# Optimization experiments

Measured on AMD Instinct MI355X. Metric: run time of the kernel, lower is better.

## Reference

```python
import jax, jax.numpy as jnp
import numpy as np

B, S, D, H, FF = 2, 2048, 1024, 16, 4096
DK = D // H
EPS = 1e-6  # LayerNormalization eps


def setup_inputs() -> dict:
    key = jax.random.key(0)
    ks = jax.random.split(key, 12)
    n = lambda k, shp, s=0.02: (jax.random.normal(k, shp, jnp.float32) * s)
    z = lambda shp: jnp.zeros(shp, jnp.float32)
    return {
        "x": jax.random.normal(ks[0], (B, S, D), jnp.float32),
        # attention projections (torch Linear: weight [out, in], bias [out])
        "wq": n(ks[1], (D, D)), "bq": z((D,)),
        "wk": n(ks[2], (D, D)), "bk": z((D,)),
        "wv": n(ks[3], (D, D)), "bv": z((D,)),
        "wo": n(ks[4], (D, D)), "bo": z((D,)),
        # feed-forward
        "w1": n(ks[5], (FF, D)), "b1": z((FF,)),
        "w2": n(ks[6], (D, FF)), "b2": z((D,)),
        # custom LayerNormalization: scalar alpha (ones(1)) and bias (zeros(1))
        "ln1_a": jnp.ones((1,), jnp.float32), "ln1_b": z((1,)),
        "ln2_a": jnp.ones((1,), jnp.float32), "ln2_b": z((1,)),
        # original code path uses `if mask:` -> falsy None; represented as 0
        "src_mask": 0,
    }


def _layernorm(x, alpha, bias):
    # Faithful to source: alpha * (x - mean) / sqrt(std + eps) + bias,
    # with std the UNBIASED std (torch default) and sqrt applied to std itself.
    mean = jnp.mean(x, axis=-1, keepdims=True)
    std = jnp.std(x, axis=-1, keepdims=True, ddof=1)
    return alpha * (x - mean) / jnp.sqrt(std + EPS) + bias


def _mha(x, wq, bq, wk, bk, wv, bv, wo, bo):
    # x: (B, S, D)
    q = (jnp.einsum("bsd,ed->bse", x, wq) + bq).reshape(B, S, H, DK).transpose(0, 2, 1, 3)
    k = (jnp.einsum("bsd,ed->bse", x, wk) + bk).reshape(B, S, H, DK).transpose(0, 2, 1, 3)
    v = (jnp.einsum("bsd,ed->bse", x, wv) + bv).reshape(B, S, H, DK).transpose(0, 2, 1, 3)
    scores = jnp.einsum("bhqd,bhkd->bhqk", q, k) / jnp.sqrt(jnp.float32(DK))
    attn = jax.nn.softmax(scores, axis=-1)  # mask is None, dropout eval -> identity
    out = jnp.einsum("bhqk,bhkd->bhqd", attn, v)
    out = out.transpose(0, 2, 1, 3).reshape(B, S, D)
    return jnp.einsum("bsd,ed->bse", out, wo) + bo


def reference(x, wq, bq, wk, bk, wv, bv, wo, bo, w1, b1, w2, b2,
              ln1_a, ln1_b, ln2_a, ln2_b, src_mask):
    # residual 1: pre-norm self-attention
    h = x + _mha(_layernorm(x, ln1_a, ln1_b), wq, bq, wk, bk, wv, bv, wo, bo)
    # residual 2: pre-norm FFN (linear -> relu -> linear)
    hn = _layernorm(h, ln2_a, ln2_b)
    ffn = jnp.einsum("bsf,df->bsd", jax.nn.relu(jnp.einsum("bsd,fd->bsf", hn, w1) + b1), w2) + b2
    return h + ffn
```

## Files before the change

kernel.cpp:

```cpp
#include <hip/hip_runtime.h>
#include <stdint.h>

#define Bb 2
#define Ss 2048
#define Dd 1024
#define Hh 16
#define DKk 64
#define FFf 4096
#define Mm 4096
#define LN_EPS 1e-6f
#define QB 32
#define KVB 64

typedef __attribute__((ext_vector_type(8))) short bf16x8;
typedef __attribute__((ext_vector_type(4))) float f32x4;

__device__ __forceinline__ unsigned short f32_to_bf16(float f) {
  union { float f; uint32_t u; } v; v.f = f;
  uint32_t u = v.u;
  u += 0x7FFFu + ((u >> 16) & 1u);
  return (unsigned short)(u >> 16);
}

struct CastArgs {
  const float4* src[6];
  ushort4* dst[6];
  int cum[7];
};
__global__ __launch_bounds__(256) void cast_all(CastArgs a, int total4) {
  int stride = gridDim.x * blockDim.x;
  for (int i = blockIdx.x * blockDim.x + threadIdx.x; i < total4; i += stride) {
    int s = 0;
    #pragma unroll
    for (int k = 1; k < 6; ++k) s += (i >= a.cum[k]);
    float4 v = a.src[s][i - a.cum[s]];
    ushort4 o;
    o.x = f32_to_bf16(v.x); o.y = f32_to_bf16(v.y);
    o.z = f32_to_bf16(v.z); o.w = f32_to_bf16(v.w);
    a.dst[s][i - a.cum[s]] = o;
  }
}

__global__ __launch_bounds__(256) void layernorm_kernel(
    const float* __restrict__ x, const float* __restrict__ alpha_p,
    const float* __restrict__ bias_p, unsigned short* __restrict__ out)
{
  __shared__ float redS[4], redQ[4];
  int row = blockIdx.x, tid = threadIdx.x;
  const float4 v = ((const float4*)(x + (size_t)row * Dd))[tid];
  float s  = v.x + v.y + v.z + v.w;
  float sq = v.x*v.x + v.y*v.y + v.z*v.z + v.w*v.w;
  #pragma unroll
  for (int off = 32; off; off >>= 1) { s += __shfl_down(s, off); sq += __shfl_down(sq, off); }
  if ((tid & 63) == 0) { redS[tid >> 6] = s; redQ[tid >> 6] = sq; }
  __syncthreads();
  float S  = redS[0] + redS[1] + redS[2] + redS[3];
  float Qq = redQ[0] + redQ[1] + redQ[2] + redQ[3];
  float mean = S * (1.f / Dd);
  float var  = fmaxf((Qq - mean * S) * (1.f / (Dd - 1)), 0.f);
  float k    = alpha_p[0] / sqrtf(sqrtf(var) + LN_EPS);
  float bias = bias_p[0];
  ushort4 ov;
  ov.x = f32_to_bf16((v.x - mean) * k + bias);
  ov.y = f32_to_bf16((v.y - mean) * k + bias);
  ov.z = f32_to_bf16((v.z - mean) * k + bias);
  ov.w = f32_to_bf16((v.w - mean) * k + bias);
  ((ushort4*)(out + (size_t)row * Dd))[tid] = ov;
}

template<int FLAGS>
__global__ __launch_bounds__(256) void gemm_bt(
    const unsigned short* __restrict__ A,
    const unsigned short* __restrict__ W,
    const float* __restrict__ bias,
    const float* __restrict__ resid,
    void* __restrict__ Cout,
    int M, int N, int K)
{
  __shared__ unsigned short As[128 * 32];
  __shared__ unsigned short Bs[128 * 32];
  const int tid  = threadIdx.x;
  const int lane = tid & 63;
  const int wid  = tid >> 6;
  const int wr   = wid >> 1, wc = wid & 1;
  const int brow = blockIdx.y * 128;
  const int bcol = blockIdx.x * 128;
  const int lane15 = lane & 15;
  const int laneK8 = (lane >> 4) * 8;

  f32x4 acc[4][4] = {};

  for (int kk = 0; kk < K; kk += 32) {
    #pragma unroll
    for (int rnd = 0; rnd < 2; ++rnd) {
      int f   = rnd * 4096 + tid * 16;
      int row = f >> 6;
      int ce  = (f & 63) >> 1;
      const unsigned short* ga = A + (size_t)(brow + row) * K + kk + ce;
      const unsigned short* gw = W + (size_t)(bcol + row) * K + kk + ce;
      __builtin_amdgcn_global_load_lds((const __attribute__((address_space(1))) void*)ga,
          (__attribute__((address_space(3))) void*)&As[rnd * 2048 + wid * 512], 16, 0, 0);
      __builtin_amdgcn_global_load_lds((const __attribute__((address_space(1))) void*)gw,
          (__attribute__((address_space(3))) void*)&Bs[rnd * 2048 + wid * 512], 16, 0, 0);
    }
    __syncthreads();

    bf16x8 af[4], bfr[4];
    #pragma unroll
    for (int i = 0; i < 4; ++i) {
      af[i]  = *(const bf16x8*)&As[(wr * 64 + i * 16 + lane15) * 32 + laneK8];
      bfr[i] = *(const bf16x8*)&Bs[(wc * 64 + i * 16 + lane15) * 32 + laneK8];
    }
    #pragma unroll
    for (int i = 0; i < 4; ++i)
      #pragma unroll
      for (int j = 0; j < 4; ++j)
        acc[i][j] = __builtin_amdgcn_mfma_f32_16x16x32_bf16(af[i], bfr[j], acc[i][j], 0, 0, 0);
    __syncthreads();
  }

  #pragma unroll
  for (int i = 0; i < 4; ++i) {
    int row0 = brow + wr * 64 + i * 16 + (lane >> 4) * 4;
    #pragma unroll
    for (int j = 0; j < 4; ++j) {
      int col = bcol + wc * 64 + j * 16 + lane15;
      float bv = bias[col];
      #pragma unroll
      for (int r = 0; r < 4; ++r) {
        float v = acc[i][j][r] + bv;
        if (FLAGS & 1) v = fmaxf(v, 0.f);
        size_t idx = (size_t)(row0 + r) * N + col;
        if (FLAGS & 2) ((float*)Cout)[idx] = resid[idx] + v;
        else           ((unsigned short*)Cout)[idx] = f32_to_bf16(v);
      }
    }
  }
}

template<int FLAGS>
__global__ __launch_bounds__(256) void gemm_bt64(
    const unsigned short* __restrict__ A,
    const unsigned short* __restrict__ W,
    const float* __restrict__ bias,
    const float* __restrict__ resid,
    void* __restrict__ Cout,
    int M, int N, int K)
{
  __shared__ unsigned short As[64 * 64];
  __shared__ unsigned short Bs[128 * 64];
  const int tid  = threadIdx.x;
  const int lane = tid & 63;
  const int wid  = tid >> 6;
  const int wr   = wid >> 1, wc = wid & 1;
  const int brow = blockIdx.y * 64;
  const int bcol = blockIdx.x * 128;
  const int lane15 = lane & 15;
  const int lgb16  = (lane >> 4) * 16;

  f32x4 acc[2][4] = {};

  for (int kk = 0; kk < K; kk += 64) {
    #pragma unroll
    for (int rnd = 0; rnd < 2; ++rnd) {
      int p    = rnd * 4096 + tid * 16;
      int row  = p >> 7;
      int colu = ((p & 127) ^ ((row & 7) << 4)) >> 1;
      const unsigned short* ga = A + (size_t)(brow + row) * K + kk + colu;
      __builtin_amdgcn_global_load_lds((const __attribute__((address_space(1))) void*)ga,
          (__attribute__((address_space(3))) void*)&As[rnd * 2048 + wid * 512], 16, 0, 0);
    }
    #pragma unroll
    for (int rnd = 0; rnd < 4; ++rnd) {
      int p    = rnd * 4096 + tid * 16;
      int row  = p >> 7;
      int colu = ((p & 127) ^ ((row & 7) << 4)) >> 1;
      const unsigned short* gw = W + (size_t)(bcol + row) * K + kk + colu;
      __builtin_amdgcn_global_load_lds((const __attribute__((address_space(1))) void*)gw,
          (__attribute__((address_space(3))) void*)&Bs[rnd * 2048 + wid * 512], 16, 0, 0);
    }
    __syncthreads();

    #pragma unroll
    for (int z = 0; z < 2; ++z) {
      bf16x8 af[2], bfr[4];
      #pragma unroll
      for (int i = 0; i < 2; ++i) {
        int r = wr * 32 + i * 16 + lane15;
        af[i] = *(const bf16x8*)((const char*)As + (r << 7) + ((z * 64 + lgb16) ^ ((r & 7) << 4)));
      }
      #pragma unroll
      for (int j = 0; j < 4; ++j) {
        int r = wc * 64 + j * 16 + lane15;
        bfr[j] = *(const bf16x8*)((const char*)Bs + (r << 7) + ((z * 64 + lgb16) ^ ((r & 7) << 4)));
      }
      #pragma unroll
      for (int i = 0; i < 2; ++i)
        #pragma unroll
        for (int j = 0; j < 4; ++j)
          acc[i][j] = __builtin_amdgcn_mfma_f32_16x16x32_bf16(af[i], bfr[j], acc[i][j], 0, 0, 0);
    }
    __syncthreads();
  }

  #pragma unroll
  for (int i = 0; i < 2; ++i) {
    int row0 = brow + wr * 32 + i * 16 + (lane >> 4) * 4;
    #pragma unroll
    for (int j = 0; j < 4; ++j) {
      int col = bcol + wc * 64 + j * 16 + lane15;
      float bv = bias[col];
      #pragma unroll
      for (int r = 0; r < 4; ++r) {
        float v = acc[i][j][r] + bv;
        if (FLAGS & 1) v = fmaxf(v, 0.f);
        size_t idx = (size_t)(row0 + r) * N + col;
        if (FLAGS & 2) ((float*)Cout)[idx] = resid[idx] + v;
        else           ((unsigned short*)Cout)[idx] = f32_to_bf16(v);
      }
    }
  }
}

__global__ __launch_bounds__(256) void gemm_qkv(
    const unsigned short* __restrict__ A,
    const unsigned short* __restrict__ W,
    const float* __restrict__ bq, const float* __restrict__ bk, const float* __restrict__ bv,
    unsigned short* __restrict__ Qb, unsigned short* __restrict__ Kb,
    unsigned short* __restrict__ Vt)
{
  const int K = Dd;
  __shared__ unsigned short As[128 * 32];
  __shared__ unsigned short Bs[128 * 32];
  const int tid  = threadIdx.x;
  const int lane = tid & 63;
  const int wid  = tid >> 6;
  const int wr   = wid >> 1, wc = wid & 1;
  const int brow = blockIdx.y * 128;
  const int bcol = blockIdx.x * 128;
  const int lane15 = lane & 15;
  const int laneK8 = (lane >> 4) * 8;

  f32x4 acc[4][4] = {};

  for (int kk = 0; kk < K; kk += 32) {
    #pragma unroll
    for (int rnd = 0; rnd < 2; ++rnd) {
      int f   = rnd * 4096 + tid * 16;
      int row = f >> 6;
      int ce  = (f & 63) >> 1;
      const unsigned short* ga = A + (size_t)(brow + row) * K + kk + ce;
      const unsigned short* gw = W + (size_t)(bcol + row) * K + kk + ce;
      __builtin_amdgcn_global_load_lds((const __attribute__((address_space(1))) void*)ga,
          (__attribute__((address_space(3))) void*)&As[rnd * 2048 + wid * 512], 16, 0, 0);
      __builtin_amdgcn_global_load_lds((const __attribute__((address_space(1))) void*)gw,
          (__attribute__((address_space(3))) void*)&Bs[rnd * 2048 + wid * 512], 16, 0, 0);
    }
    __syncthreads();

    bf16x8 af[4], bfr[4];
    #pragma unroll
    for (int i = 0; i < 4; ++i) {
      af[i]  = *(const bf16x8*)&As[(wr * 64 + i * 16 + lane15) * 32 + laneK8];
      bfr[i] = *(const bf16x8*)&Bs[(wc * 64 + i * 16 + lane15) * 32 + laneK8];
    }
    #pragma unroll
    for (int i = 0; i < 4; ++i)
      #pragma unroll
      for (int j = 0; j < 4; ++j)
        acc[i][j] = __builtin_amdgcn_mfma_f32_16x16x32_bf16(af[i], bfr[j], acc[i][j], 0, 0, 0);
    __syncthreads();
  }

  const int region = bcol >> 10;
  const float* bp = (region == 0) ? bq : (region == 1) ? bk : bv;

  #pragma unroll
  for (int i = 0; i < 4; ++i) {
    int row0 = brow + wr * 64 + i * 16 + (lane >> 4) * 4;
    #pragma unroll
    for (int j = 0; j < 4; ++j) {
      int col = bcol + wc * 64 + j * 16 + lane15;
      int cl  = col & 1023;
      float bvv = bp[cl];
      if (region < 2) {
        unsigned short* dst = (region == 0) ? Qb : Kb;
        #pragma unroll
        for (int r = 0; r < 4; ++r)
          dst[(size_t)(row0 + r) * Dd + cl] = f32_to_bf16(acc[i][j][r] + bvv);
      } else {
        ushort4 pk;
        pk.x = f32_to_bf16(acc[i][j][0] + bvv);
        pk.y = f32_to_bf16(acc[i][j][1] + bvv);
        pk.z = f32_to_bf16(acc[i][j][2] + bvv);
        pk.w = f32_to_bf16(acc[i][j][3] + bvv);
        int bidx = row0 >> 11;
        int s0   = row0 & (Ss - 1);
        *(ushort4*)(Vt + ((size_t)(bidx * Dd + cl)) * Ss + s0) = pk;
      }
    }
  }
}

__global__ __launch_bounds__(128) void attn_mfma(
    const unsigned short* __restrict__ Q,
    const unsigned short* __restrict__ K,
    const unsigned short* __restrict__ Vt,
    unsigned short* __restrict__ ctx)
{
  __shared__ unsigned short Ks[KVB * 64];
  __shared__ unsigned short Vs[64 * KVB];
  __shared__ unsigned short Ps[2][16 * 64];

  const int tid  = threadIdx.x;
  const int lane = tid & 63;
  const int wid  = tid >> 6;
  const int l15  = lane & 15;
  const int lg   = lane >> 4;
  const int b    = blockIdx.y >> 4, h = blockIdx.y & 15;
  const int q0   = blockIdx.x * QB + wid * 16;

  const size_t qkbase = (size_t)b * Ss * Dd + (size_t)h * DKk;
  const size_t vtbase = ((size_t)b * Dd + h * DKk) * (size_t)Ss;
  const float KLOG = 0.125f * 1.44269504f;

  bf16x8 qf[2];
  #pragma unroll
  for (int z = 0; z < 2; ++z)
    qf[z] = *(const bf16x8*)(Q + qkbase + (size_t)(q0 + l15) * Dd + z * 32 + lg * 8);

  f32x4 acc_o[4] = {};
  float mrow[4], lrow[4];
  #pragma unroll
  for (int ri = 0; ri < 4; ++ri) { mrow[ri] = -1e30f; lrow[ri] = 0.f; }

  for (int kt = 0; kt < Ss; kt += KVB) {
    #pragma unroll
    for (int rnd = 0; rnd < 4; ++rnd) {
      int p    = rnd * 2048 + tid * 16;
      int row  = p >> 7;
      int colu = ((p & 127) ^ ((row & 7) << 4)) >> 1;
      const unsigned short* gk = K  + qkbase + (size_t)(kt + row) * Dd + colu;
      const unsigned short* gv = Vt + vtbase + (size_t)row * Ss + kt + colu;
      __builtin_amdgcn_global_load_lds((const __attribute__((address_space(1))) void*)gk,
          (__attribute__((address_space(3))) void*)&Ks[rnd * 1024 + wid * 512], 16, 0, 0);
      __builtin_amdgcn_global_load_lds((const __attribute__((address_space(1))) void*)gv,
          (__attribute__((address_space(3))) void*)&Vs[rnd * 1024 + wid * 512], 16, 0, 0);
    }
    __syncthreads();

    f32x4 accs[4] = {};
    #pragma unroll
    for (int cf = 0; cf < 4; ++cf) {
      int r = cf * 16 + l15;
      int rsw = (r & 7) << 4;
      #pragma unroll
      for (int z = 0; z < 2; ++z) {
        const bf16x8 kf = *(const bf16x8*)((const char*)Ks + (r << 7) + ((z * 64 + lg * 16) ^ rsw));
        accs[cf] = __builtin_amdgcn_mfma_f32_16x16x32_bf16(qf[z], kf, accs[cf], 0, 0, 0);
      }
    }

    float tmv[4];
    #pragma unroll
    for (int ri = 0; ri < 4; ++ri) {
      float t = fmaxf(fmaxf(accs[0][ri], accs[1][ri]), fmaxf(accs[2][ri], accs[3][ri]));
      t = fmaxf(t, __shfl_xor(t, 1));
      t = fmaxf(t, __shfl_xor(t, 2));
      t = fmaxf(t, __shfl_xor(t, 4));
      t = fmaxf(t, __shfl_xor(t, 8));
      tmv[ri] = t;
    }
    bool need = false;
    #pragma unroll
    for (int ri = 0; ri < 4; ++ri) need |= (tmv[ri] > mrow[ri] + 64.f);
    if (__any(need)) {
      #pragma unroll
      for (int ri = 0; ri < 4; ++ri) {
        float mn = fmaxf(mrow[ri], tmv[ri]);
        float sc = __builtin_amdgcn_exp2f((mrow[ri] - mn) * KLOG);
        lrow[ri] *= sc;
        #pragma unroll
        for (int cf = 0; cf < 4; ++cf) acc_o[cf][ri] *= sc;
        mrow[ri] = mn;
      }
    }
    #pragma unroll
    for (int ri = 0; ri < 4; ++ri) {
      float mk = mrow[ri] * KLOG;
      float pv[4], rs = 0.f;
      #pragma unroll
      for (int cf = 0; cf < 4; ++cf) {
        pv[cf] = __builtin_amdgcn_exp2f(__builtin_fmaf(accs[cf][ri], KLOG, -mk));
        rs += pv[cf];
      }
      rs += __shfl_xor(rs, 1);
      rs += __shfl_xor(rs, 2);
      rs += __shfl_xor(rs, 4);
      rs += __shfl_xor(rs, 8);
      lrow[ri] += rs;
      int prow = lg * 4 + ri;
      int psw  = (prow & 7) << 4;
      char* pb = (char*)&Ps[wid][0] + (prow << 7);
      #pragma unroll
      for (int cf = 0; cf < 4; ++cf)
        *(unsigned short*)(pb + ((cf * 32 + l15 * 2) ^ psw)) =
            (unsigned short)(__float_as_uint(pv[cf]) >> 16);
    }

    #pragma unroll
    for (int kc = 0; kc < 2; ++kc) {
      int r = l15;
      const bf16x8 pf = *(const bf16x8*)((const char*)&Ps[wid][0] + (r << 7) + ((kc * 64 + lg * 16) ^ ((r & 7) << 4)));
      #pragma unroll
      for (int cf = 0; cf < 4; ++cf) {
        int vr = cf * 16 + l15;
        const bf16x8 vf = *(const bf16x8*)((const char*)Vs + (vr << 7) + ((kc * 64 + lg * 16) ^ ((vr & 7) << 4)));
        acc_o[cf] = __builtin_amdgcn_mfma_f32_16x16x32_bf16(pf, vf, acc_o[cf], 0, 0, 0);
      }
    }
    __syncthreads();
  }

  #pragma unroll
  for (int ri = 0; ri < 4; ++ri) {
    float inv = 1.f / lrow[ri];
    int q = q0 + lg * 4 + ri;
    #pragma unroll
    for (int cf = 0; cf < 4; ++cf)
      ctx[qkbase + (size_t)q * Dd + cf * 16 + l15] = f32_to_bf16(acc_o[cf][ri] * inv);
  }
}

extern "C" void kernel_launch(void* const* d_in, const int* in_sizes, int n_in,
                              void* d_out, int out_size, void* d_ws, size_t ws_size,
                              hipStream_t stream)
{
  const float* x    = (const float*)d_in[0];
  const float* wq   = (const float*)d_in[1];
  const float* bq   = (const float*)d_in[2];
  const float* wk   = (const float*)d_in[3];
  const float* bk   = (const float*)d_in[4];
  const float* wv   = (const float*)d_in[5];
  const float* bv   = (const float*)d_in[6];
  const float* wo   = (const float*)d_in[7];
  const float* bo   = (const float*)d_in[8];
  const float* w1   = (const float*)d_in[9];
  const float* b1   = (const float*)d_in[10];
  const float* w2   = (const float*)d_in[11];
  const float* b2   = (const float*)d_in[12];
  const float* ln1a = (const float*)d_in[13];
  const float* ln1b = (const float*)d_in[14];
  const float* ln2a = (const float*)d_in[15];
  const float* ln2b = (const float*)d_in[16];

  char* ws = (char*)d_ws;
  const size_t MB = 1u << 20;
  unsigned short* wqkv_b = (unsigned short*)(ws + 0 * MB);
  unsigned short* wo_b   = (unsigned short*)(ws + 6 * MB);
  unsigned short* w1_b   = (unsigned short*)(ws + 8 * MB);
  unsigned short* w2_b   = (unsigned short*)(ws + 16 * MB);
  unsigned short* xn1    = (unsigned short*)(ws + 24 * MB);
  unsigned short* Qb     = (unsigned short*)(ws + 32 * MB);
  unsigned short* Kb     = (unsigned short*)(ws + 40 * MB);
  unsigned short* Vt     = (unsigned short*)(ws + 48 * MB);
  unsigned short* ctx    = (unsigned short*)(ws + 56 * MB);
  float*          h      = (float*)(ws + 64 * MB);
  unsigned short* hn2    = (unsigned short*)(ws + 80 * MB);
  unsigned short* f1     = (unsigned short*)(ws + 88 * MB);
  float* out = (float*)d_out;

  {
    const int DD4 = (Dd * Dd) >> 2;
    const int FD4 = (FFf * Dd) >> 2;
    CastArgs a;
    a.src[0] = (const float4*)wq; a.src[1] = (const float4*)wk; a.src[2] = (const float4*)wv;
    a.src[3] = (const float4*)wo; a.src[4] = (const float4*)w1; a.src[5] = (const float4*)w2;
    a.dst[0] = (ushort4*)wqkv_b;
    a.dst[1] = (ushort4*)(wqkv_b + 1 * Dd * Dd);
    a.dst[2] = (ushort4*)(wqkv_b + 2 * Dd * Dd);
    a.dst[3] = (ushort4*)wo_b;
    a.dst[4] = (ushort4*)w1_b;
    a.dst[5] = (ushort4*)w2_b;
    a.cum[0] = 0;
    a.cum[1] = DD4; a.cum[2] = 2 * DD4; a.cum[3] = 3 * DD4; a.cum[4] = 4 * DD4;
    a.cum[5] = 4 * DD4 + FD4; a.cum[6] = 4 * DD4 + 2 * FD4;
    cast_all<<<2048, 256, 0, stream>>>(a, a.cum[6]);
  }

  layernorm_kernel<<<Mm, 256, 0, stream>>>(x, ln1a, ln1b, xn1);
  gemm_qkv<<<dim3(3 * Dd / 128, Mm / 128), 256, 0, stream>>>(xn1, wqkv_b, bq, bk, bv, Qb, Kb, Vt);
  attn_mfma<<<dim3(Ss / QB, Bb * Hh), 128, 0, stream>>>(Qb, Kb, Vt, ctx);
  gemm_bt64<2><<<dim3(Dd / 128, Mm / 64), 256, 0, stream>>>(ctx, wo_b, bo, x, h, Mm, Dd, Dd);
  layernorm_kernel<<<Mm, 256, 0, stream>>>(h, ln2a, ln2b, hn2);
  gemm_bt<1><<<dim3(FFf / 128, Mm / 128), 256, 0, stream>>>(hn2, w1_b, b1, nullptr, f1, Mm, FFf, Dd);
  gemm_bt64<2><<<dim3(Dd / 128, Mm / 64), 256, 0, stream>>>(f1, w2_b, b2, h, out, Mm, Dd, FFf);
}
```

Measured before the change: 437.3 us.

## Double-buffer LDS tiles in all GEMMs and attention; widen attention blocks

Each GEMM kernel and the attention kernel now keep two LDS buffers, so the next K/V or A/W tile is fetched asynchronously while the current tile feeds MFMA, hiding global-load latency behind compute. The attention kernel also moves from 2 to 4 waves per block (QB 32 to 64, 256 threads), so each staged K/V tile is shared by more query rows. In exchange LDS use per block doubles, which may reduce occupancy, and the attention grid has half as many blocks.

```diff
diff --git a/kernel.cpp b/kernel.cpp
--- a/kernel.cpp
+++ b/kernel.cpp
@@ -9,11 +9,15 @@
 #define FFf 4096
 #define Mm 4096
 #define LN_EPS 1e-6f
-#define QB 32
+#define QB 64
 #define KVB 64
 
 typedef __attribute__((ext_vector_type(8))) short bf16x8;
 typedef __attribute__((ext_vector_type(4))) float f32x4;
+
+#define GLOAD_LDS(gptr, lptr) \
+  __builtin_amdgcn_global_load_lds((const __attribute__((address_space(1))) void*)(gptr), \
+                                   (__attribute__((address_space(3))) void*)(lptr), 16, 0, 0)
 
 __device__ __forceinline__ unsigned short f32_to_bf16(float f) {
   union { float f; uint32_t u; } v; v.f = f;
@@ -77,8 +81,8 @@
     void* __restrict__ Cout,
     int M, int N, int K)
 {
-  __shared__ unsigned short As[128 * 32];
-  __shared__ unsigned short Bs[128 * 32];
+  __shared__ unsigned short As[2][128 * 32];
+  __shared__ unsigned short Bs[2][128 * 32];
   const int tid  = threadIdx.x;
   const int lane = tid & 63;
   const int wid  = tid >> 6;
@@ -90,26 +94,28 @@
 
   f32x4 acc[4][4] = {};
 
-  for (int kk = 0; kk < K; kk += 32) {
+  auto STAGE = [&](int kk2, int bufi) {
     #pragma unroll
     for (int rnd = 0; rnd < 2; ++rnd) {
       int f   = rnd * 4096 + tid * 16;
       int row = f >> 6;
       int ce  = (f & 63) >> 1;
-      const unsigned short* ga = A + (size_t)(brow + row) * K + kk + ce;
-      const unsigned short* gw = W + (size_t)(bcol + row) * K + kk + ce;
-      __builtin_amdgcn_global_load_lds((const __attribute__((address_space(1))) void*)ga,
-          (__attribute__((address_space(3))) void*)&As[rnd * 2048 + wid * 512], 16, 0, 0);
-      __builtin_amdgcn_global_load_lds((const __attribute__((address_space(1))) void*)gw,
-          (__attribute__((address_space(3))) void*)&Bs[rnd * 2048 + wid * 512], 16, 0, 0);
-    }
-    __syncthreads();
+      GLOAD_LDS(A + (size_t)(brow + row) * K + kk2 + ce, &As[bufi][rnd * 2048 + wid * 512]);
+      GLOAD_LDS(W + (size_t)(bcol + row) * K + kk2 + ce, &Bs[bufi][rnd * 2048 + wid * 512]);
+    }
+  };
+
+  STAGE(0, 0);
+  __syncthreads();
+  int cur = 0;
+  for (int kk = 0; kk < K; kk += 32) {
+    if (kk + 32 < K) STAGE(kk + 32, cur ^ 1);
 
     bf16x8 af[4], bfr[4];
     #pragma unroll
     for (int i = 0; i < 4; ++i) {
-      af[i]  = *(const bf16x8*)&As[(wr * 64 + i * 16 + lane15) * 32 + laneK8];
-      bfr[i] = *(const bf16x8*)&Bs[(wc * 64 + i * 16 + lane15) * 32 + laneK8];
+      af[i]  = *(const bf16x8*)&As[cur][(wr * 64 + i * 16 + lane15) * 32 + laneK8];
+      bfr[i] = *(const bf16x8*)&Bs[cur][(wc * 64 + i * 16 + lane15) * 32 + laneK8];
     }
     #pragma unroll
     for (int i = 0; i < 4; ++i)
@@ -117,6 +123,7 @@
       for (int j = 0; j < 4; ++j)
         acc[i][j] = __builtin_amdgcn_mfma_f32_16x16x32_bf16(af[i], bfr[j], acc[i][j], 0, 0, 0);
     __syncthreads();
+    cur ^= 1;
   }
 
   #pragma unroll
@@ -147,8 +154,8 @@
     void* __restrict__ Cout,
     int M, int N, int K)
 {
-  __shared__ unsigned short As[64 * 64];
-  __shared__ unsigned short Bs[128 * 64];
+  __shared__ unsigned short As[2][64 * 64];
+  __shared__ unsigned short Bs[2][128 * 64];
   const int tid  = threadIdx.x;
   const int lane = tid & 63;
   const int wid  = tid >> 6;
@@ -160,26 +167,28 @@
 
   f32x4 acc[2][4] = {};
 
-  for (int kk = 0; kk < K; kk += 64) {
+  auto STAGE = [&](int kk2, int bufi) {
     #pragma unroll
     for (int rnd = 0; rnd < 2; ++rnd) {
       int p    = rnd * 4096 + tid * 16;
       int row  = p >> 7;
       int colu = ((p & 127) ^ ((row & 7) << 4)) >> 1;
-      const unsigned short* ga = A + (size_t)(brow + row) * K + kk + colu;
-      __builtin_amdgcn_global_load_lds((const __attribute__((address_space(1))) void*)ga,
-          (__attribute__((address_space(3))) void*)&As[rnd * 2048 + wid * 512], 16, 0, 0);
+      GLOAD_LDS(A + (size_t)(brow + row) * K + kk2 + colu, &As[bufi][rnd * 2048 + wid * 512]);
     }
     #pragma unroll
     for (int rnd = 0; rnd < 4; ++rnd) {
       int p    = rnd * 4096 + tid * 16;
       int row  = p >> 7;
       int colu = ((p & 127) ^ ((row & 7) << 4)) >> 1;
-      const unsigned short* gw = W + (size_t)(bcol + row) * K + kk + colu;
-      __builtin_amdgcn_global_load_lds((const __attribute__((address_space(1))) void*)gw,
-          (__attribute__((address_space(3))) void*)&Bs[rnd * 2048 + wid * 512], 16, 0, 0);
-    }
-    __syncthreads();
+      GLOAD_LDS(W + (size_t)(bcol + row) * K + kk2 + colu, &Bs[bufi][rnd * 2048 + wid * 512]);
+    }
+  };
+
+  STAGE(0, 0);
+  __syncthreads();
+  int cur = 0;
+  for (int kk = 0; kk < K; kk += 64) {
+    if (kk + 64 < K) STAGE(kk + 64, cur ^ 1);
 
     #pragma unroll
     for (int z = 0; z < 2; ++z) {
@@ -187,12 +196,12 @@
       #pragma unroll
       for (int i = 0; i < 2; ++i) {
         int r = wr * 32 + i * 16 + lane15;
-        af[i] = *(const bf16x8*)((const char*)As + (r << 7) + ((z * 64 + lgb16) ^ ((r & 7) << 4)));
+        af[i] = *(const bf16x8*)((const char*)&As[cur][0] + (r << 7) + ((z * 64 + lgb16) ^ ((r & 7) << 4)));
       }
       #pragma unroll
       for (int j = 0; j < 4; ++j) {
         int r = wc * 64 + j * 16 + lane15;
-        bfr[j] = *(const bf16x8*)((const char*)Bs + (r << 7) + ((z * 64 + lgb16) ^ ((r & 7) << 4)));
+        bfr[j] = *(const bf16x8*)((const char*)&Bs[cur][0] + (r << 7) + ((z * 64 + lgb16) ^ ((r & 7) << 4)));
       }
       #pragma unroll
       for (int i = 0; i < 2; ++i)
@@ -201,6 +210,7 @@
           acc[i][j] = __builtin_amdgcn_mfma_f32_16x16x32_bf16(af[i], bfr[j], acc[i][j], 0, 0, 0);
     }
     __syncthreads();
+    cur ^= 1;
   }
 
   #pragma unroll
@@ -230,8 +240,8 @@
     unsigned short* __restrict__ Vt)
 {
   const int K = Dd;
-  __shared__ unsigned short As[128 * 32];
-  __shared__ unsigned short Bs[128 * 32];
+  __shared__ unsigned short As[2][128 * 32];
+  __shared__ unsigned short Bs[2][128 * 32];
   const int tid  = threadIdx.x;
   const int lane = tid & 63;
   const int wid  = tid >> 6;
@@ -243,26 +253,28 @@
 
   f32x4 acc[4][4] = {};
 
-  for (int kk = 0; kk < K; kk += 32) {
+  auto STAGE = [&](int kk2, int bufi) {
     #pragma unroll
     for (int rnd = 0; rnd < 2; ++rnd) {
       int f   = rnd * 4096 + tid * 16;
       int row = f >> 6;
       int ce  = (f & 63) >> 1;
-      const unsigned short* ga = A + (size_t)(brow + row) * K + kk + ce;
-      const unsigned short* gw = W + (size_t)(bcol + row) * K + kk + ce;
-      __builtin_amdgcn_global_load_lds((const __attribute__((address_space(1))) void*)ga,
-          (__attribute__((address_space(3))) void*)&As[rnd * 2048 + wid * 512], 16, 0, 0);
-      __builtin_amdgcn_global_load_lds((const __attribute__((address_space(1))) void*)gw,
-          (__attribute__((address_space(3))) void*)&Bs[rnd * 2048 + wid * 512], 16, 0, 0);
-    }
-    __syncthreads();
+      GLOAD_LDS(A + (size_t)(brow + row) * K + kk2 + ce, &As[bufi][rnd * 2048 + wid * 512]);
+      GLOAD_LDS(W + (size_t)(bcol + row) * K + kk2 + ce, &Bs[bufi][rnd * 2048 + wid * 512]);
+    }
+  };
+
+  STAGE(0, 0);
+  __syncthreads();
+  int cur = 0;
+  for (int kk = 0; kk < K; kk += 32) {
+    if (kk + 32 < K) STAGE(kk + 32, cur ^ 1);
 
     bf16x8 af[4], bfr[4];
     #pragma unroll
     for (int i = 0; i < 4; ++i) {
-      af[i]  = *(const bf16x8*)&As[(wr * 64 + i * 16 + lane15) * 32 + laneK8];
-      bfr[i] = *(const bf16x8*)&Bs[(wc * 64 + i * 16 + lane15) * 32 + laneK8];
+      af[i]  = *(const bf16x8*)&As[cur][(wr * 64 + i * 16 + lane15) * 32 + laneK8];
+      bfr[i] = *(const bf16x8*)&Bs[cur][(wc * 64 + i * 16 + lane15) * 32 + laneK8];
     }
     #pragma unroll
     for (int i = 0; i < 4; ++i)
@@ -270,6 +282,7 @@
       for (int j = 0; j < 4; ++j)
         acc[i][j] = __builtin_amdgcn_mfma_f32_16x16x32_bf16(af[i], bfr[j], acc[i][j], 0, 0, 0);
     __syncthreads();
+    cur ^= 1;
   }
 
   const int region = bcol >> 10;
@@ -302,15 +315,15 @@
   }
 }
 
-__global__ __launch_bounds__(128) void attn_mfma(
+__global__ __launch_bounds__(256) void attn_mfma(
     const unsigned short* __restrict__ Q,
     const unsigned short* __restrict__ K,
     const unsigned short* __restrict__ Vt,
     unsigned short* __restrict__ ctx)
 {
-  __shared__ unsigned short Ks[KVB * 64];
-  __shared__ unsigned short Vs[64 * KVB];
-  __shared__ unsigned short Ps[2][16 * 64];
+  __shared__ unsigned short Ks[2][KVB * 64];
+  __shared__ unsigned short Vs[2][64 * KVB];
+  __shared__ unsigned short Ps[4][16 * 64];
 
   const int tid  = threadIdx.x;
   const int lane = tid & 63;
@@ -334,29 +347,33 @@
   #pragma unroll
   for (int ri = 0; ri < 4; ++ri) { mrow[ri] = -1e30f; lrow[ri] = 0.f; }
 
-  for (int kt = 0; kt < Ss; kt += KVB) {
-    #pragma unroll
-    for (int rnd = 0; rnd < 4; ++rnd) {
-      int p    = rnd * 2048 + tid * 16;
+  auto STAGE = [&](int kt2, int bufi) {
+    #pragma unroll
+    for (int rnd = 0; rnd < 2; ++rnd) {
+      int p    = rnd * 4096 + tid * 16;
       int row  = p >> 7;
       int colu = ((p & 127) ^ ((row & 7) << 4)) >> 1;
-      const unsigned short* gk = K  + qkbase + (size_t)(kt + row) * Dd + colu;
-      const unsigned short* gv = Vt + vtbase + (size_t)row * Ss + kt + colu;
-      __builtin_amdgcn_global_load_lds((const __attribute__((address_space(1))) void*)gk,
-          (__attribute__((address_space(3))) void*)&Ks[rnd * 1024 + wid * 512], 16, 0, 0);
-      __builtin_amdgcn_global_load_lds((const __attribute__((address_space(1))) void*)gv,
-          (__attribute__((address_space(3))) void*)&Vs[rnd * 1024 + wid * 512], 16, 0, 0);
-    }
-    __syncthreads();
+      GLOAD_LDS(K  + qkbase + (size_t)(kt2 + row) * Dd + colu, &Ks[bufi][rnd * 2048 + wid * 512]);
+      GLOAD_LDS(Vt + vtbase + (size_t)row * Ss + kt2 + colu,   &Vs[bufi][rnd * 2048 + wid * 512]);
+    }
+  };
+
+  STAGE(0, 0);
+  __syncthreads();
+  int cur = 0;
+
+  for (int kt = 0; kt < Ss; kt += KVB) {
+    if (kt + KVB < Ss) STAGE(kt + KVB, cur ^ 1);
 
     f32x4 accs[4] = {};
+    const char* kb = (const char*)&Ks[cur][0];
     #pragma unroll
     for (int cf = 0; cf < 4; ++cf) {
       int r = cf * 16 + l15;
       int rsw = (r & 7) << 4;
       #pragma unroll
       for (int z = 0; z < 2; ++z) {
-        const bf16x8 kf = *(const bf16x8*)((const char*)Ks + (r << 7) + ((z * 64 + lg * 16) ^ rsw));
+        const bf16x8 kf = *(const bf16x8*)(kb + (r << 7) + ((z * 64 + lg * 16) ^ rsw));
         accs[cf] = __builtin_amdgcn_mfma_f32_16x16x32_bf16(qf[z], kf, accs[cf], 0, 0, 0);
       }
     }
@@ -408,6 +425,7 @@
             (unsigned short)(__float_as_uint(pv[cf]) >> 16);
     }
 
+    const char* vb = (const char*)&Vs[cur][0];
     #pragma unroll
     for (int kc = 0; kc < 2; ++kc) {
       int r = l15;
@@ -415,11 +433,12 @@
       #pragma unroll
       for (int cf = 0; cf < 4; ++cf) {
         int vr = cf * 16 + l15;
-        const bf16x8 vf = *(const bf16x8*)((const char*)Vs + (vr << 7) + ((kc * 64 + lg * 16) ^ ((vr & 7) << 4)));
+        const bf16x8 vf = *(const bf16x8*)(vb + (vr << 7) + ((kc * 64 + lg * 16) ^ ((vr & 7) << 4)));
         acc_o[cf] = __builtin_amdgcn_mfma_f32_16x16x32_bf16(pf, vf, acc_o[cf], 0, 0, 0);
       }
     }
     __syncthreads();
+    cur ^= 1;
   }
 
   #pragma unroll
@@ -490,7 +509,7 @@
 
   layernorm_kernel<<<Mm, 256, 0, stream>>>(x, ln1a, ln1b, xn1);
   gemm_qkv<<<dim3(3 * Dd / 128, Mm / 128), 256, 0, stream>>>(xn1, wqkv_b, bq, bk, bv, Qb, Kb, Vt);
-  attn_mfma<<<dim3(Ss / QB, Bb * Hh), 128, 0, stream>>>(Qb, Kb, Vt, ctx);
+  attn_mfma<<<dim3(Ss / QB, Bb * Hh), 256, 0, stream>>>(Qb, Kb, Vt, ctx);
   gemm_bt64<2><<<dim3(Dd / 128, Mm / 64), 256, 0, stream>>>(ctx, wo_b, bo, x, h, Mm, Dd, Dd);
   layernorm_kernel<<<Mm, 256, 0, stream>>>(h, ln2a, ln2b, hn2);
   gemm_bt<1><<<dim3(FFf / 128, Mm / 128), 256, 0, stream>>>(hn2, w1_b, b1, nullptr, f1, Mm, FFf, Dd);
```

Result: faster. 407.3 us (-6.9%).
